# Optimization experiments

Measured on AMD Instinct MI355X. Metric: run time of the kernel, lower is better.

Reference implementation:

```python
import jax, jax.numpy as jnp
import numpy as np

BETA = 0.9       # membrane decay
THR = 1.0        # snntorch Leaky default threshold
SLOPE = 25.0     # fast_sigmoid surrogate slope (forward-only here)


def _heaviside(x):
    return (x > 0).astype(x.dtype)


def setup_inputs() -> dict:
    key = jax.random.key(0)
    ks = jax.random.split(key, 4)
    B, D, H1, H2, C = 4096, 1024, 2048, 1024, 64
    x = jax.random.normal(ks[0], (B, D), jnp.float32)
    W1 = jax.random.normal(ks[1], (H1, D), jnp.float32) * 0.02
    b1 = jnp.zeros((H1,), jnp.float32)
    W2 = jax.random.normal(ks[2], (H2, H1), jnp.float32) * 0.02
    b2 = jnp.zeros((H2,), jnp.float32)
    Wo = jax.random.normal(ks[3], (C, H2), jnp.float32) * 0.02
    bo = jnp.zeros((C,), jnp.float32)
    return {"x": x, "W1": W1, "b1": b1, "W2": W2, "b2": b2,
            "Wo": Wo, "bo": bo, "num_steps": 20}


def reference(x, W1, b1, W2, b2, Wo, bo, num_steps):
    B = x.shape[0]
    mem1 = jnp.zeros((B, W1.shape[0]), x.dtype)
    mem2 = jnp.zeros((B, W2.shape[0]), x.dtype)
    spk_sum = jnp.zeros((B, W2.shape[0]), x.dtype)

    def step(carry, _):
        cur, m1, m2, ss = carry
        # Layer 1: Linear + Leaky (reset-by-subtraction, persistent mem)
        h1 = cur @ W1.T + b1                      # [B, H1]
        r1 = _heaviside(m1 - THR)                 # reset from previous mem
        m1 = BETA * m1 + h1 - r1 * THR
        s1 = _heaviside(m1 - THR)
        # Layer 2: Linear + Leaky
        h2 = s1 @ W2.T + b2                       # [B, H2]
        r2 = _heaviside(m2 - THR)
        m2 = BETA * m2 + h2 - r2 * THR
        s2 = _heaviside(m2 - THR)
        # NOTE: s2 feeds back into layer-1 Linear next step (cur = x only at t=0)
        return (s2, m1, m2, ss + s2), None

    (cur, mem1, mem2, spk_sum), _ = jax.lax.scan(
        step, (x, mem1, mem2, spk_sum), None, length=num_steps)
    return (spk_sum / num_steps) @ Wo.T + bo
```

## Files before the change

### kernel.cpp

```cpp
#include <hip/hip_runtime.h>
#include <hip/hip_bf16.h>

#define B_   4096
#define D_   1024
#define H1_  2048
#define H2_  1024
#define C_   64

typedef double d4 __attribute__((ext_vector_type(4)));

#if defined(__has_builtin)
#  if __has_builtin(__builtin_amdgcn_mfma_f64_16x16x4f64)
#    define MFMA64(A, B, C) __builtin_amdgcn_mfma_f64_16x16x4f64((A), (B), (C), 0, 0, 0)
#    define HAVE_MFMA64 1
#  elif __has_builtin(__builtin_amdgcn_mfma_f64_16x16x4_f64)
#    define MFMA64(A, B, C) __builtin_amdgcn_mfma_f64_16x16x4_f64((A), (B), (C), 0, 0, 0)
#    define HAVE_MFMA64 1
#  endif
#endif

__global__ void k_probe(int* flag) {
#if defined(HAVE_MFMA64)
    int lane = threadIdx.x & 63;
    int lr = lane & 15, lk = lane >> 4;
    double a  = (double)(5 * lr + 3 * lk + 1);
    double bb = (double)(11 * lk + 2 * lr + 2);
    d4 c = {0.0, 0.0, 0.0, 0.0};
    c = MFMA64(a, bb, c);
    int okm[4] = {1, 1, 1, 1};
#pragma unroll
    for (int j = 0; j < 4; ++j) {
        double e1 = 0, e2 = 0, e3 = 0, e4 = 0;
        for (int k = 0; k < 4; ++k) {
            e1 += (double)(5 * (4 * lk + j) + 3 * k + 1) * (double)(11 * k + 2 * lr + 2);
            e2 += (double)(5 * lr + 3 * k + 1) * (double)(11 * k + 2 * (4 * lk + j) + 2);
            e3 += (double)(5 * (lk + 4 * j) + 3 * k + 1) * (double)(11 * k + 2 * lr + 2);
            e4 += (double)(5 * lr + 3 * k + 1) * (double)(11 * k + 2 * (lk + 4 * j) + 2);
        }
        if (c[j] != e1) okm[0] = 0;
        if (c[j] != e2) okm[1] = 0;
        if (c[j] != e3) okm[2] = 0;
        if (c[j] != e4) okm[3] = 0;
    }
    int f = 0;
    for (int m = 3; m >= 0; --m) {
        unsigned long long all = __ballot(okm[m] != 0);
        if (all == ~0ULL) f = m + 1;
    }
    if (lane == 0) flag[0] = f;
#else
    if ((threadIdx.x & 63) == 0) flag[0] = 0;
#endif
}

__global__ __launch_bounds__(256) void k_transpose(const float* __restrict__ in,
                                                   float* __restrict__ out,
                                                   int R, int C) {
    __shared__ float t[32][33];
    int c0 = blockIdx.x * 32;
    int r0 = blockIdx.y * 32;
    int lx = threadIdx.x;
    int ly = threadIdx.y;
#pragma unroll
    for (int q = 0; q < 4; ++q) {
        int rr = ly + 8 * q;
        t[rr][lx] = in[(size_t)(r0 + rr) * C + (c0 + lx)];
    }
    __syncthreads();
#pragma unroll
    for (int q = 0; q < 4; ++q) {
        int cc = ly + 8 * q;
        out[(size_t)(c0 + cc) * R + (r0 + lx)] = t[lx][cc];
    }
}

#define GBM 128
#define GBN 128
#define GBK 16
#define LDP 136
__global__ __launch_bounds__(512, 4) void k_gemm_mfma(const float* __restrict__ x,
                                                      const float* __restrict__ W1,
                                                      const float* __restrict__ b1,
                                                      double* __restrict__ m1out,
                                                      const int* __restrict__ flag) {
#if defined(HAVE_MFMA64)
    int fm = flag[0];
    if (fm < 1 || fm > 4) return;
    __shared__ float As[GBK][LDP];
    __shared__ float Bs[GBK][LDP];

    int tid = threadIdx.x;
    int m0 = blockIdx.x * GBM;
    int n0 = blockIdx.y * GBN;
    int w = tid >> 6, lane = tid & 63;
    int wr = w >> 2;
    int wc = w & 3;
    int lr = lane & 15, lk = lane >> 4;
    int srow = tid >> 2;
    int skq = (tid & 3) * 4;

    d4 acc[4][2];
#pragma unroll
    for (int i = 0; i < 4; ++i)
#pragma unroll
        for (int j = 0; j < 2; ++j) acc[i][j] = (d4){0.0, 0.0, 0.0, 0.0};

    for (int k0 = 0; k0 < D_; k0 += GBK) {
        float4 av = *(const float4*)&x [(size_t)(m0 + srow) * D_ + k0 + skq];
        float4 bv = *(const float4*)&W1[(size_t)(n0 + srow) * D_ + k0 + skq];
        __syncthreads();
        As[skq + 0][srow] = av.x;
        As[skq + 1][srow] = av.y;
        As[skq + 2][srow] = av.z;
        As[skq + 3][srow] = av.w;
        Bs[skq + 0][srow] = bv.x;
        Bs[skq + 1][srow] = bv.y;
        Bs[skq + 2][srow] = bv.z;
        Bs[skq + 3][srow] = bv.w;
        __syncthreads();
#pragma unroll
        for (int kb = 0; kb < 4; ++kb) {
            double a[4], bfr[2];
#pragma unroll
            for (int i = 0; i < 4; ++i)
                a[i] = (double)As[kb * 4 + lk][wr * 64 + 16 * i + lr];
#pragma unroll
            for (int j = 0; j < 2; ++j)
                bfr[j] = (double)Bs[kb * 4 + lk][wc * 32 + 16 * j + lr];
#pragma unroll
            for (int i = 0; i < 4; ++i)
#pragma unroll
                for (int j = 0; j < 2; ++j)
                    acc[i][j] = MFMA64(a[i], bfr[j], acc[i][j]);
        }
    }
#pragma unroll
    for (int j = 0; j < 2; ++j)
#pragma unroll
        for (int i = 0; i < 4; ++i)
#pragma unroll
            for (int r = 0; r < 4; ++r) {
                int rin = (fm == 1) ? (4 * lk + r) : (fm == 2) ? lr
                        : (fm == 3) ? (lk + 4 * r) : lr;
                int cin = (fm == 1) ? lr : (fm == 2) ? (4 * lk + r)
                        : (fm == 3) ? lr : (lk + 4 * r);
                int row = m0 + wr * 64 + 16 * i + rin;
                int col = n0 + wc * 32 + 16 * j + cin;
                m1out[(size_t)row * H1_ + col] = acc[i][j][r] + (double)b1[col];
            }
#else
    (void)x; (void)W1; (void)b1; (void)m1out; (void)flag;
#endif
}

#define BM 128
#define BN 128
#define BK 8
__global__ __launch_bounds__(256) void k_gemm1(const float* __restrict__ x,
                                               const float* __restrict__ W1,
                                               const float* __restrict__ b1,
                                               double* __restrict__ m1out,
                                               const int* __restrict__ flag) {
    int fm = flag[0];
    if (fm >= 1 && fm <= 4) return;
    __shared__ double As[BK][BM + 4];
    __shared__ double Bs[BK][BN + 4];

    int tid = threadIdx.x;
    int m0 = blockIdx.x * BM;
    int n0 = blockIdx.y * BN;
    int tx = tid & 15;
    int ty = tid >> 4;
    int lr = tid >> 1;
    int lk = (tid & 1) * 4;

    double acc[8][8] = {};

    for (int k0 = 0; k0 < D_; k0 += BK) {
        float4 av = *(const float4*)&x [(size_t)(m0 + lr) * D_ + k0 + lk];
        float4 bv = *(const float4*)&W1[(size_t)(n0 + lr) * D_ + k0 + lk];
        __syncthreads();
        As[lk + 0][lr] = (double)av.x;
        As[lk + 1][lr] = (double)av.y;
        As[lk + 2][lr] = (double)av.z;
        As[lk + 3][lr] = (double)av.w;
        Bs[lk + 0][lr] = (double)bv.x;
        Bs[lk + 1][lr] = (double)bv.y;
        Bs[lk + 2][lr] = (double)bv.z;
        Bs[lk + 3][lr] = (double)bv.w;
        __syncthreads();
#pragma unroll
        for (int kk = 0; kk < BK; ++kk) {
            double a[8], b[8];
#pragma unroll
            for (int i = 0; i < 8; ++i) a[i] = As[kk][tx + 16 * i];
#pragma unroll
            for (int j = 0; j < 8; ++j) b[j] = Bs[kk][ty + 16 * j];
#pragma unroll
            for (int i = 0; i < 8; ++i)
#pragma unroll
                for (int j = 0; j < 8; ++j)
                    acc[i][j] += a[i] * b[j];
        }
    }
#pragma unroll
    for (int j = 0; j < 8; ++j) {
        double bj = (double)b1[n0 + ty + 16 * j];
#pragma unroll
        for (int i = 0; i < 8; ++i) {
            m1out[(size_t)(m0 + tx + 16 * i) * H1_ + (n0 + ty + 16 * j)] =
                acc[i][j] + bj;
        }
    }
}

__global__ __launch_bounds__(256) void k_snn(const double* __restrict__ m1_0,
                                             const float* __restrict__ b1,
                                             const float* __restrict__ W1T,
                                             const float* __restrict__ W2T,
                                             const float* __restrict__ b2,
                                             const float* __restrict__ Wo,
                                             const float* __restrict__ bo,
                                             const int* __restrict__ nsteps_p,
                                             float* __restrict__ out) {
    __shared__ __align__(16) double pjbuf[H2_];
    __shared__ __align__(16) int l2idx[H2_];
    __shared__ unsigned long long s1by[32];
    __shared__ unsigned long long s2nb[32];
    __shared__ int ncnt[2];
    __shared__ int anyb1[4], anyb2[4];

    int* l1idx = (int*)pjbuf;

    int b = blockIdx.x;
    int tid = threadIdx.x;
    int lane = tid & 63;
    int wv = tid >> 6;
    int T = nsteps_p[0];

    double m1r[8], m2r[4];
    float b1f[8], b2f[4];
    int cnt[4];

    const double* m1p = m1_0 + (size_t)b * H1_ + 8 * tid;
    {
        double2 v0 = *(const double2*)(m1p + 0);
        double2 v1 = *(const double2*)(m1p + 2);
        double2 v2 = *(const double2*)(m1p + 4);
        double2 v3 = *(const double2*)(m1p + 6);
        m1r[0] = v0.x; m1r[1] = v0.y; m1r[2] = v1.x; m1r[3] = v1.y;
        m1r[4] = v2.x; m1r[5] = v2.y; m1r[6] = v3.x; m1r[7] = v3.y;
    }
    {
        float4 f0 = *(const float4*)(b1 + 8 * tid);
        float4 f1 = *(const float4*)(b1 + 8 * tid + 4);
        b1f[0] = f0.x; b1f[1] = f0.y; b1f[2] = f0.z; b1f[3] = f0.w;
        b1f[4] = f1.x; b1f[5] = f1.y; b1f[6] = f1.z; b1f[7] = f1.w;
        float4 f2 = *(const float4*)(b2 + 4 * tid);
        b2f[0] = f2.x; b2f[1] = f2.y; b2f[2] = f2.z; b2f[3] = f2.w;
    }
#pragma unroll
    for (int q = 0; q < 4; ++q) { m2r[q] = 0.0; cnt[q] = 0; }

    int anyS2 = 0;

#define ACC2(v) { m2r[0] += (double)(v).x; m2r[1] += (double)(v).y; \
                  m2r[2] += (double)(v).z; m2r[3] += (double)(v).w; }

    for (int t = 0; t < T; ++t) {
        if (t > 0) {
#pragma unroll
            for (int q = 0; q < 8; ++q)
                m1r[q] = 0.9 * m1r[q] - (m1r[q] > 1.0 ? 1.0 : 0.0) + (double)b1f[q];
            if (anyS2) {
                int n2 = ncnt[1];
                const char* Wc = (const char*)W1T;
                size_t toff = (size_t)tid << 5;
                for (int k2 = 0; k2 < n2; ++k2) {
                    const float4* c4 = (const float4*)(Wc + l2idx[k2] + toff);
                    float4 va = c4[0];
                    float4 vb = c4[1];
                    m1r[0] += (double)va.x; m1r[1] += (double)va.y;
                    m1r[2] += (double)va.z; m1r[3] += (double)va.w;
                    m1r[4] += (double)vb.x; m1r[5] += (double)vb.y;
                    m1r[6] += (double)vb.z; m1r[7] += (double)vb.w;
                }
            }
        }
        unsigned bflag = 0;
#pragma unroll
        for (int q = 0; q < 8; ++q) bflag |= (m1r[q] > 1.0 ? 1u : 0u) << q;
        ((unsigned char*)s1by)[tid] = (unsigned char)bflag;
        {
            int wa = __any((int)bflag);
            if (lane == 0) anyb1[wv] = wa;
        }
#pragma unroll
        for (int q = 0; q < 4; ++q)
            m2r[q] = 0.9 * m2r[q] - (m2r[q] > 1.0 ? 1.0 : 0.0) + (double)b2f[q];
        {
            unsigned nib = 0;
#pragma unroll
            for (int q = 0; q < 4; ++q) nib |= (m2r[q] > 1.0 ? 1u : 0u) << q;
            ((unsigned char*)s2nb)[tid] = (unsigned char)nib;
            int wa = __any((int)nib);
            if (lane == 0) anyb2[wv] = wa;
        }
        __syncthreads();
        int any1 = anyb1[0] | anyb1[1] | anyb1[2] | anyb1[3];
        if (any1) {
            if (tid < 64) {
                unsigned long long bits = (tid < 32) ? s1by[tid] : 0ULL;
                int pc = __popcll(bits);
                int sc = pc;
#pragma unroll
                for (int d = 1; d < 64; d <<= 1) {
                    int o = __shfl_up(sc, d);
                    if (tid >= d) sc += o;
                }
                if (tid == 63) ncnt[0] = sc;
                int off = sc - pc;
                int base = tid << 6;
                while (bits) {
                    l1idx[off++] = (base + __builtin_ctzll(bits)) << 12;
                    bits &= bits - 1;
                }
            }
            __syncthreads();
            {
                int n1 = ncnt[0];
                const char* Wc = (const char*)W2T;
                size_t toff = (size_t)tid << 4;
                int k = 0;
                for (; k + 8 <= n1; k += 8) {
                    int4 oa = *(const int4*)&l1idx[k];
                    int4 ob = *(const int4*)&l1idx[k + 4];
                    float4 v0 = *(const float4*)(Wc + oa.x + toff);
                    float4 v1 = *(const float4*)(Wc + oa.y + toff);
                    float4 v2 = *(const float4*)(Wc + oa.z + toff);
                    float4 v3 = *(const float4*)(Wc + oa.w + toff);
                    float4 v4 = *(const float4*)(Wc + ob.x + toff);
                    float4 v5 = *(const float4*)(Wc + ob.y + toff);
                    float4 v6 = *(const float4*)(Wc + ob.z + toff);
                    float4 v7 = *(const float4*)(Wc + ob.w + toff);
                    ACC2(v0); ACC2(v1); ACC2(v2); ACC2(v3);
                    ACC2(v4); ACC2(v5); ACC2(v6); ACC2(v7);
                }
                for (; k < n1; ++k) {
                    float4 v = *(const float4*)(Wc + l1idx[k] + toff);
                    ACC2(v);
                }
            }
            {
                unsigned nib = 0;
#pragma unroll
                for (int q = 0; q < 4; ++q) nib |= (m2r[q] > 1.0 ? 1u : 0u) << q;
                ((unsigned char*)s2nb)[tid] = (unsigned char)nib;
                int wa = __any((int)nib);
                if (lane == 0) anyb2[wv] = wa;
            }
            __syncthreads();
        }
        anyS2 = anyb2[0] | anyb2[1] | anyb2[2] | anyb2[3];
#pragma unroll
        for (int q = 0; q < 4; ++q) cnt[q] += (m2r[q] > 1.0) ? 1 : 0;
        if (anyS2) {
            if (tid < 64) {
                unsigned long long wbits = 0ULL;
                if (tid < 16) {
                    unsigned long long w0 = s2nb[2 * tid];
                    unsigned long long w1 = s2nb[2 * tid + 1];
                    w0 &= 0x0F0F0F0F0F0F0F0FULL;
                    w0 = (w0 | (w0 >> 4)) & 0x00FF00FF00FF00FFULL;
                    w0 = (w0 | (w0 >> 8)) & 0x0000FFFF0000FFFFULL;
                    w0 = (w0 | (w0 >> 16)) & 0x00000000FFFFFFFFULL;
                    w1 &= 0x0F0F0F0F0F0F0F0FULL;
                    w1 = (w1 | (w1 >> 4)) & 0x00FF00FF00FF00FFULL;
                    w1 = (w1 | (w1 >> 8)) & 0x0000FFFF0000FFFFULL;
                    w1 = (w1 | (w1 >> 16)) & 0x00000000FFFFFFFFULL;
                    wbits = w0 | (w1 << 32);
                }
                int pc = __popcll(wbits);
                int sc = pc;
#pragma unroll
                for (int d = 1; d < 64; d <<= 1) {
                    int o = __shfl_up(sc, d);
                    if (tid >= d) sc += o;
                }
                if (tid == 63) ncnt[1] = sc;
                int off = sc - pc;
                int base = tid << 6;
                while (wbits) {
                    l2idx[off++] = (base + __builtin_ctzll(wbits)) << 13;
                    wbits &= wbits - 1;
                }
            }
            __syncthreads();
        }
    }
#undef ACC2

    __syncthreads();
#pragma unroll
    for (int q = 0; q < 4; ++q)
        pjbuf[4 * tid + q] = (double)cnt[q] / (double)T;
    {
        unsigned nib = 0;
#pragma unroll
        for (int q = 0; q < 4; ++q) nib |= (cnt[q] > 0 ? 1u : 0u) << q;
        ((unsigned char*)s2nb)[tid] = (unsigned char)nib;
    }
    __syncthreads();
    if (tid < 64) {
        unsigned long long wbits = 0ULL;
        if (tid < 16) {
            unsigned long long w0 = s2nb[2 * tid];
            unsigned long long w1 = s2nb[2 * tid + 1];
            w0 &= 0x0F0F0F0F0F0F0F0FULL;
            w0 = (w0 | (w0 >> 4)) & 0x00FF00FF00FF00FFULL;
            w0 = (w0 | (w0 >> 8)) & 0x0000FFFF0000FFFFULL;
            w0 = (w0 | (w0 >> 16)) & 0x00000000FFFFFFFFULL;
            w1 &= 0x0F0F0F0F0F0F0F0FULL;
            w1 = (w1 | (w1 >> 4)) & 0x00FF00FF00FF00FFULL;
            w1 = (w1 | (w1 >> 8)) & 0x0000FFFF0000FFFFULL;
            w1 = (w1 | (w1 >> 16)) & 0x00000000FFFFFFFFULL;
            wbits = w0 | (w1 << 32);
        }
        int pc = __popcll(wbits);
        int sc = pc;
#pragma unroll
        for (int d = 1; d < 64; d <<= 1) {
            int o = __shfl_up(sc, d);
            if (tid >= d) sc += o;
        }
        if (tid == 63) ncnt[1] = sc;
        int off = sc - pc;
        int base = tid << 6;
        while (wbits) {
            l2idx[off++] = base + __builtin_ctzll(wbits);
            wbits &= wbits - 1;
        }
    }
    __syncthreads();
    if (tid < C_) {
        int c = tid;
        int na = ncnt[1];
        const float* worow = &Wo[(size_t)c * H2_];
        double acc = 0.0;
        for (int k = 0; k < na; ++k) {
            int j = l2idx[k];
            acc += pjbuf[j] * (double)worow[j];
        }
        out[(size_t)b * C_ + c] = (float)(acc + (double)bo[c]);
    }
}

extern "C" void kernel_launch(void* const* d_in, const int* in_sizes, int n_in,
                              void* d_out, int out_size, void* d_ws, size_t ws_size,
                              hipStream_t stream) {
    const float* x  = (const float*)d_in[0];
    const float* W1 = (const float*)d_in[1];
    const float* b1 = (const float*)d_in[2];
    const float* W2 = (const float*)d_in[3];
    const float* b2 = (const float*)d_in[4];
    const float* Wo = (const float*)d_in[5];
    const float* bo = (const float*)d_in[6];
    const int* nst  = (const int*)d_in[7];
    float* out = (float*)d_out;

    size_t off_m1   = 0;
    size_t off_w1t  = off_m1 + (size_t)B_ * H1_ * 8;
    size_t off_w2t  = off_w1t + (size_t)D_ * H1_ * 4;
    size_t off_flag = off_w2t + (size_t)H1_ * H2_ * 4;
    size_t need     = off_flag + 64;
    if (ws_size < need) return;

    double* m1ws = (double*)((char*)d_ws + off_m1);
    float*  W1T  = (float*)((char*)d_ws + off_w1t);
    float*  W2T  = (float*)((char*)d_ws + off_w2t);
    int*    flag = (int*)((char*)d_ws + off_flag);

    k_probe<<<1, 64, 0, stream>>>(flag);

    k_transpose<<<dim3(D_ / 32, H1_ / 32), dim3(32, 8), 0, stream>>>(W1, W1T, H1_, D_);
    k_transpose<<<dim3(H1_ / 32, H2_ / 32), dim3(32, 8), 0, stream>>>(W2, W2T, H2_, H1_);

    k_gemm_mfma<<<dim3(B_ / GBM, H1_ / GBN), 512, 0, stream>>>(x, W1, b1, m1ws, flag);
    k_gemm1<<<dim3(B_ / BM, H1_ / BN), 256, 0, stream>>>(x, W1, b1, m1ws, flag);

    k_snn<<<B_, 256, 0, stream>>>(m1ws, b1, W1T, W2T, b2, Wo, bo, nst, out);
}
```

Baseline: 446.4 us.

## Shrink MFMA GEMM tile to 128x64 with padded double shared-memory staging

Measured after the change: 451.1 us. No clear change (+1.0%).

```diff
diff --git a/kernel.cpp b/kernel.cpp
--- a/kernel.cpp
+++ b/kernel.cpp
@@ -75,10 +75,17 @@
 }
 
 #define GBM 128
-#define GBN 128
+#define GBN 64
 #define GBK 16
-#define LDP 136
-__global__ __launch_bounds__(512, 4) void k_gemm_mfma(const float* __restrict__ x,
+#define ASZ64 2192
+#define BSZ64 1168
+__device__ __forceinline__ int AIDX64(int k, int r) {
+    return k * 136 + ((k >> 2) << 3) + r;
+}
+__device__ __forceinline__ int BIDX64(int k, int r) {
+    return k * 72 + ((k >> 2) << 3) + r;
+}
+__global__ __launch_bounds__(512, 8) void k_gemm_mfma(const float* __restrict__ x,
                                                       const float* __restrict__ W1,
                                                       const float* __restrict__ b1,
                                                       double* __restrict__ m1out,
@@ -86,65 +93,80 @@
 #if defined(HAVE_MFMA64)
     int fm = flag[0];
     if (fm < 1 || fm > 4) return;
-    __shared__ float As[GBK][LDP];
-    __shared__ float Bs[GBK][LDP];
+    __shared__ double As[ASZ64];
+    __shared__ double Bs[BSZ64];
 
     int tid = threadIdx.x;
     int m0 = blockIdx.x * GBM;
     int n0 = blockIdx.y * GBN;
     int w = tid >> 6, lane = tid & 63;
-    int wr = w >> 2;
-    int wc = w & 3;
+    int wr = w >> 1;
+    int wc = w & 1;
     int lr = lane & 15, lk = lane >> 4;
-    int srow = tid >> 2;
-    int skq = (tid & 3) * 4;
-
-    d4 acc[4][2];
-#pragma unroll
-    for (int i = 0; i < 4; ++i)
+
+    int srowA = tid >> 2;
+    int gA    = tid & 3;
+    int woffA = AIDX64(gA * 4, srowA);
+
+    int srowB = (tid & 255) >> 2;
+    int gB    = tid & 3;
+    int woffB = BIDX64(gB * 4, srowB);
+    bool doB  = (tid < 256);
+
+    const float* xrow = x  + (size_t)(m0 + srowA) * D_;
+    const float* wrow = W1 + (size_t)(n0 + srowB) * D_;
+
+    d4 acc[2][2];
+#pragma unroll
+    for (int i = 0; i < 2; ++i)
 #pragma unroll
         for (int j = 0; j < 2; ++j) acc[i][j] = (d4){0.0, 0.0, 0.0, 0.0};
 
     for (int k0 = 0; k0 < D_; k0 += GBK) {
-        float4 av = *(const float4*)&x [(size_t)(m0 + srow) * D_ + k0 + skq];
-        float4 bv = *(const float4*)&W1[(size_t)(n0 + srow) * D_ + k0 + skq];
+        float4 av = *(const float4*)&xrow[k0 + gA * 4];
+        float4 bv;
+        if (doB) bv = *(const float4*)&wrow[k0 + gB * 4];
         __syncthreads();
-        As[skq + 0][srow] = av.x;
-        As[skq + 1][srow] = av.y;
-        As[skq + 2][srow] = av.z;
-        As[skq + 3][srow] = av.w;
-        Bs[skq + 0][srow] = bv.x;
-        Bs[skq + 1][srow] = bv.y;
-        Bs[skq + 2][srow] = bv.z;
-        Bs[skq + 3][srow] = bv.w;
+        As[woffA +   0] = (double)av.x;
+        As[woffA + 136] = (double)av.y;
+        As[woffA + 272] = (double)av.z;
+        As[woffA + 408] = (double)av.w;
+        if (doB) {
+            Bs[woffB +   0] = (double)bv.x;
+            Bs[woffB +  72] = (double)bv.y;
+            Bs[woffB + 144] = (double)bv.z;
+            Bs[woffB + 216] = (double)bv.w;
+        }
         __syncthreads();
 #pragma unroll
         for (int kb = 0; kb < 4; ++kb) {
-            double a[4], bfr[2];
-#pragma unroll
-            for (int i = 0; i < 4; ++i)
-                a[i] = (double)As[kb * 4 + lk][wr * 64 + 16 * i + lr];
-#pragma unroll
-            for (int j = 0; j < 2; ++j)
-                bfr[j] = (double)Bs[kb * 4 + lk][wc * 32 + 16 * j + lr];
-#pragma unroll
-            for (int i = 0; i < 4; ++i)
+            int k = kb * 4 + lk;
+            int abase = AIDX64(k, wr * 32 + lr);
+            int bbase = BIDX64(k, wc * 32 + lr);
+            double a[2], bfr[2];
+#pragma unroll
+            for (int i = 0; i < 2; ++i) a[i]   = As[abase + 16 * i];
+#pragma unroll
+            for (int j = 0; j < 2; ++j) bfr[j] = Bs[bbase + 16 * j];
+#pragma unroll
+            for (int i = 0; i < 2; ++i)
 #pragma unroll
                 for (int j = 0; j < 2; ++j)
                     acc[i][j] = MFMA64(a[i], bfr[j], acc[i][j]);
         }
     }
+
 #pragma unroll
     for (int j = 0; j < 2; ++j)
 #pragma unroll
-        for (int i = 0; i < 4; ++i)
+        for (int i = 0; i < 2; ++i)
 #pragma unroll
             for (int r = 0; r < 4; ++r) {
                 int rin = (fm == 1) ? (4 * lk + r) : (fm == 2) ? lr
                         : (fm == 3) ? (lk + 4 * r) : lr;
                 int cin = (fm == 1) ? lr : (fm == 2) ? (4 * lk + r)
                         : (fm == 3) ? lr : (lk + 4 * r);
-                int row = m0 + wr * 64 + 16 * i + rin;
+                int row = m0 + wr * 32 + 16 * i + rin;
                 int col = n0 + wc * 32 + 16 * j + cin;
                 m1out[(size_t)row * H1_ + col] = acc[i][j][r] + (double)b1[col];
             }
```
